# Kernel optimization log

Measured on AMD Instinct MI355X. Metric: run time of the kernel, lower is better.

The kernel has to match this reference:

```python
import jax, jax.numpy as jnp
import numpy as np

B, C, H, W, N = 16, 81, 128, 128, 64


def setup_inputs() -> dict:
    key = jax.random.key(0)
    k1, k2, k3, k4, k5 = jax.random.split(key, 5)
    bbox_pred = jax.random.normal(k1, (B, 4, H, W), jnp.float32)
    class_pred = jax.random.normal(k2, (B, C, H, W), jnp.float32)
    # well-formed GT boxes in [0,1]: x1y1 + positive wh
    xy = jax.random.uniform(k3, (B, N, 2), jnp.float32)
    wh = jax.random.uniform(k4, (B, N, 2), jnp.float32) * 0.5 + 0.05
    boxes = jnp.concatenate([xy, xy + wh], axis=-1)  # [B,N,4]
    labels = jax.random.randint(k5, (B, N), 0, C).astype(jnp.int32)
    return {"bbox_pred": bbox_pred, "class_pred": class_pred,
            "boxes": boxes, "labels": labels}


def reference(bbox_pred, class_pred, boxes, labels):
    Bb, Cc, Hh, Ww = class_pred.shape
    A = Hh * Ww
    pb = bbox_pred.transpose(0, 2, 3, 1).reshape(Bb, A, 4)   # [B,A,4]
    pc = class_pred.transpose(0, 2, 3, 1).reshape(Bb, A, Cc)  # [B,A,C]

    # pairwise IoU [B,A,N] via broadcasting (pred [B,A,1,4] vs gt [B,1,N,4])
    p = pb[:, :, None, :]
    g = boxes[:, None, :, :]
    ix1 = jnp.maximum(p[..., 0], g[..., 0])
    iy1 = jnp.maximum(p[..., 1], g[..., 1])
    ix2 = jnp.minimum(p[..., 2], g[..., 2])
    iy2 = jnp.minimum(p[..., 3], g[..., 3])
    inter = jnp.clip(ix2 - ix1, 0) * jnp.clip(iy2 - iy1, 0)
    pa = (pb[..., 2] - pb[..., 0]) * (pb[..., 3] - pb[..., 1])      # [B,A]
    ga = (boxes[..., 2] - boxes[..., 0]) * (boxes[..., 3] - boxes[..., 1])  # [B,N]
    union = pa[:, :, None] + ga[:, None, :] - inter
    ious = inter / union

    max_ious = ious.max(axis=-1)            # [B,A]
    max_idx = jnp.argmax(ious, axis=-1)     # [B,A]
    pos = max_ious > 0.5                    # [B,A]
    posf = pos.astype(pc.dtype)
    npos = posf.sum(axis=-1)                # [B]
    denom = jnp.maximum(npos, 1.0)

    assigned_labels = jnp.take_along_axis(labels, max_idx, axis=1)          # [B,A]
    assigned_boxes = jnp.take_along_axis(boxes, max_idx[..., None], axis=1)  # [B,A,4]

    # cross-entropy per anchor (mean over positives)
    logp = jax.nn.log_softmax(pc, axis=-1)
    ce = -jnp.take_along_axis(logp, assigned_labels[..., None], axis=2)[..., 0]
    cls_loss = (ce * posf).sum(axis=-1) / denom

    # smooth-L1 (beta=1), mean over positive elements (npos*4)
    diff = pb - assigned_boxes
    ad = jnp.abs(diff)
    sl1 = jnp.where(ad < 1.0, 0.5 * diff * diff, ad - 0.5)
    reg_loss = (sl1 * posf[..., None]).sum(axis=(-1, -2)) / (denom * 4.0)

    # fallback when an image has zero positives: CE with all-zero labels
    zero_loss = -logp[..., 0].mean(axis=-1)

    per_img = jnp.where(npos > 0, cls_loss + reg_loss, zero_loss)
    return per_img.mean()
```

## Files before the change

kernel.cpp:

```cpp
#include <hip/hip_runtime.h>
#include <math.h>

#define Bc 16
#define Cc 81
#define AA 16384
#define Nn 64
#define TPB 256
#define ILP 2
#define APB (TPB * ILP)
#define BLOCKS_PER_IMG (AA / APB)
#define NBLOCKS (Bc * BLOCKS_PER_IMG)
#define G 9
#define NG 9

__global__ __launch_bounds__(TPB) void det_loss_main(
    const float* __restrict__ bbox_pred,
    const float* __restrict__ class_pred,
    const float* __restrict__ boxes,
    const int* __restrict__ labels,
    float4* __restrict__ ws_part)
{
    __shared__ float4 sbox[Nn];
    __shared__ float  sga[Nn];
    __shared__ int    slab[Nn];

    const int blk  = blockIdx.x;
    const int b    = blk / BLOCKS_PER_IMG;
    const int ablk = blk % BLOCKS_PER_IMG;
    const int t    = threadIdx.x;

    if (t < Nn) {
        float4 g = ((const float4*)boxes)[b * Nn + t];
        sbox[t] = g;
        sga[t]  = (g.z - g.x) * (g.w - g.y);
        slab[t] = labels[b * Nn + t];
    }
    __syncthreads();

    const int a0 = ablk * APB + 2 * t;

    const float* bp = bbox_pred + (size_t)b * 4 * AA + a0;
    const float2 X1 = *(const float2*)(bp + 0 * AA);
    const float2 Y1 = *(const float2*)(bp + 1 * AA);
    const float2 X2 = *(const float2*)(bp + 2 * AA);
    const float2 Y2 = *(const float2*)(bp + 3 * AA);
    const float pa_0 = (X2.x - X1.x) * (Y2.x - Y1.x);
    const float pa_1 = (X2.y - X1.y) * (Y2.y - Y1.y);

    const float* cp = class_pred + (size_t)b * Cc * AA + a0;
    float2 buf0[G], buf1[G];
#pragma unroll
    for (int k = 0; k < G; ++k) buf0[k] = *(const float2*)(cp + (size_t)k * AA);

    float best0 = -INFINITY, best1 = -INFINITY;
    int   j0 = 0, j1 = 0;
#pragma unroll 8
    for (int j = 0; j < Nn; ++j) {
        const float4 g  = sbox[j];
        const float  ga = sga[j];
        {
            const float ix1 = fmaxf(X1.x, g.x);
            const float iy1 = fmaxf(Y1.x, g.y);
            const float ix2 = fminf(X2.x, g.z);
            const float iy2 = fminf(Y2.x, g.w);
            const float inter = fmaxf(ix2 - ix1, 0.0f) * fmaxf(iy2 - iy1, 0.0f);
            const float iou = inter * __builtin_amdgcn_rcpf(pa_0 + ga - inter);
            if (iou > best0) { best0 = iou; j0 = j; }
        }
        {
            const float ix1 = fmaxf(X1.y, g.x);
            const float iy1 = fmaxf(Y1.y, g.y);
            const float ix2 = fminf(X2.y, g.z);
            const float iy2 = fminf(Y2.y, g.w);
            const float inter = fmaxf(ix2 - ix1, 0.0f) * fmaxf(iy2 - iy1, 0.0f);
            const float iou = inter * __builtin_amdgcn_rcpf(pa_1 + ga - inter);
            if (iou > best1) { best1 = iou; j1 = j; }
        }
    }
    const float posf0 = (best0 > 0.5f) ? 1.0f : 0.0f;
    const float posf1 = (best1 > 0.5f) ? 1.0f : 0.0f;
    const int    lab0 = slab[j0];
    const int    lab1 = slab[j1];
    const float4 gb0  = sbox[j0];
    const float4 gb1  = sbox[j1];

    const float xl0 = class_pred[((size_t)b * Cc + lab0) * AA + a0];
    const float xl1 = class_pred[((size_t)b * Cc + lab1) * AA + a0 + 1];

    float sA0 = 0.0f, sA1 = 0.0f, sB0 = 0.0f, sB1 = 0.0f;
    float x00 = 0.0f, x01 = 0.0f;
#pragma unroll
    for (int g = 0; g < NG; ++g) {
        if (g + 1 < NG) {
            if ((g & 1) == 0) {
#pragma unroll
                for (int k = 0; k < G; ++k)
                    buf1[k] = *(const float2*)(cp + (size_t)((g + 1) * G + k) * AA);
            } else {
#pragma unroll
                for (int k = 0; k < G; ++k)
                    buf0[k] = *(const float2*)(cp + (size_t)((g + 1) * G + k) * AA);
            }
        }
#pragma unroll
        for (int k = 0; k < G; ++k) {
            const float2 x = ((g & 1) == 0) ? buf0[k] : buf1[k];
            if (g == 0 && k == 0) { x00 = x.x; x01 = x.y; }
            if (k & 1) { sB0 += __expf(x.x); sB1 += __expf(x.y); }
            else       { sA0 += __expf(x.x); sA1 += __expf(x.y); }
        }
    }
    const float lse0 = __logf(sA0 + sB0);
    const float lse1 = __logf(sA1 + sB1);

    const float ce    = (lse0 - xl0) * posf0 + (lse1 - xl1) * posf1;
    const float logp0 = (x00 - lse0) + (x01 - lse1);

    float sl = 0.0f;
    {
        const float d0 = X1.x - gb0.x, d1 = Y1.x - gb0.y, d2 = X2.x - gb0.z, d3 = Y2.x - gb0.w;
        const float a_0 = fabsf(d0), a_1 = fabsf(d1), a_2 = fabsf(d2), a_3 = fabsf(d3);
        float s0 = 0.0f;
        s0 += (a_0 < 1.0f) ? 0.5f * d0 * d0 : a_0 - 0.5f;
        s0 += (a_1 < 1.0f) ? 0.5f * d1 * d1 : a_1 - 0.5f;
        s0 += (a_2 < 1.0f) ? 0.5f * d2 * d2 : a_2 - 0.5f;
        s0 += (a_3 < 1.0f) ? 0.5f * d3 * d3 : a_3 - 0.5f;
        sl += s0 * posf0;
    }
    {
        const float d0 = X1.y - gb1.x, d1 = Y1.y - gb1.y, d2 = X2.y - gb1.z, d3 = Y2.y - gb1.w;
        const float a_0 = fabsf(d0), a_1 = fabsf(d1), a_2 = fabsf(d2), a_3 = fabsf(d3);
        float s1 = 0.0f;
        s1 += (a_0 < 1.0f) ? 0.5f * d0 * d0 : a_0 - 0.5f;
        s1 += (a_1 < 1.0f) ? 0.5f * d1 * d1 : a_1 - 0.5f;
        s1 += (a_2 < 1.0f) ? 0.5f * d2 * d2 : a_2 - 0.5f;
        s1 += (a_3 < 1.0f) ? 0.5f * d3 * d3 : a_3 - 0.5f;
        sl += s1 * posf1;
    }

    float v0 = posf0 + posf1, v1 = ce, v2 = sl, v3 = logp0;
#pragma unroll
    for (int o = 32; o > 0; o >>= 1) {
        v0 += __shfl_down(v0, o);
        v1 += __shfl_down(v1, o);
        v2 += __shfl_down(v2, o);
        v3 += __shfl_down(v3, o);
    }
    __shared__ float4 red[4];
    const int wave = t >> 6, lane = t & 63;
    if (lane == 0) red[wave] = make_float4(v0, v1, v2, v3);
    __syncthreads();
    if (t == 0) {
        float4 r0 = red[0], r1 = red[1], r2 = red[2], r3 = red[3];
        ws_part[blk] = make_float4(r0.x + r1.x + r2.x + r3.x,
                                   r0.y + r1.y + r2.y + r3.y,
                                   r0.z + r1.z + r2.z + r3.z,
                                   r0.w + r1.w + r2.w + r3.w);
    }
}

__global__ __launch_bounds__(256) void det_loss_final(
    const float4* __restrict__ ws_part, float* __restrict__ out)
{
    const int t = threadIdx.x;
    float4 p0 = ws_part[t];
    float4 p1 = ws_part[t + 256];
#pragma unroll
    for (int o = 1; o < 32; o <<= 1) {
        p0.x += __shfl_xor(p0.x, o); p0.y += __shfl_xor(p0.y, o);
        p0.z += __shfl_xor(p0.z, o); p0.w += __shfl_xor(p0.w, o);
        p1.x += __shfl_xor(p1.x, o); p1.y += __shfl_xor(p1.y, o);
        p1.z += __shfl_xor(p1.z, o); p1.w += __shfl_xor(p1.w, o);
    }
    __shared__ float4 simg[16];
    const int lane = t & 63, w = t >> 6;
    if (lane == 0 || lane == 32) {
        const int img = 2 * w + (lane >> 5);
        simg[img]     = p0;
        simg[img + 8] = p1;
    }
    __syncthreads();
    float per = 0.0f;
    if (t < Bc) {
        const float4 s = simg[t];
        const float npos = s.x;
        const float denom = fmaxf(npos, 1.0f);
        const float cls_reg = s.y / denom + s.z / (denom * 4.0f);
        const float zero_loss = -s.w / (float)AA;
        per = (npos > 0.0f) ? cls_reg : zero_loss;
    }
#pragma unroll
    for (int o = 8; o > 0; o >>= 1) per += __shfl_down(per, o);
    if (t == 0) out[0] = per * (1.0f / (float)Bc);
}

extern "C" void kernel_launch(void* const* d_in, const int* in_sizes, int n_in,
                              void* d_out, int out_size, void* d_ws, size_t ws_size,
                              hipStream_t stream) {
    const float* bbox_pred  = (const float*)d_in[0];
    const float* class_pred = (const float*)d_in[1];
    const float* boxes      = (const float*)d_in[2];
    const int*   labels     = (const int*)d_in[3];
    float* out = (float*)d_out;
    float4* ws = (float4*)d_ws;

    det_loss_main<<<NBLOCKS, TPB, 0, stream>>>(bbox_pred, class_pred, boxes, labels, ws);
    det_loss_final<<<1, 256, 0, stream>>>(ws, out);
}
```

Measured before the change: 25.14 us.

## Triple-buffer class loads, use nontemporal loads, select label logit in-loop

Deepens the class-logit prefetch from double to triple buffering, so two groups of channel loads are in flight while the IoU loop and exp sums run. All streaming loads become nontemporal. The separate gather of the assigned-label logit is replaced by a select inside the channel loop, which removes one dependent global load after the IoU search. The cost is more VGPRs for the third buffer plus extra compare/select work per channel, which could lower occupancy.

```diff
diff --git a/kernel.cpp b/kernel.cpp
--- a/kernel.cpp
+++ b/kernel.cpp
@@ -1,17 +1,26 @@
 #include <hip/hip_runtime.h>
 #include <math.h>
+#include <string.h>
 
 #define Bc 16
 #define Cc 81
 #define AA 16384
 #define Nn 64
 #define TPB 256
-#define ILP 2
-#define APB (TPB * ILP)
+#define APB 512
 #define BLOCKS_PER_IMG (AA / APB)
 #define NBLOCKS (Bc * BLOCKS_PER_IMG)
 #define G 9
 #define NG 9
+
+#define NTL(p) __builtin_nontemporal_load(p)
+
+__device__ __forceinline__ float2 ntl2(const float* p) {
+    const double d = __builtin_nontemporal_load((const double*)p);
+    float2 r;
+    memcpy(&r, &d, 8);
+    return r;
+}
 
 __global__ __launch_bounds__(TPB) void det_loss_main(
     const float* __restrict__ bbox_pred,
@@ -40,17 +49,19 @@
     const int a0 = ablk * APB + 2 * t;
 
     const float* bp = bbox_pred + (size_t)b * 4 * AA + a0;
-    const float2 X1 = *(const float2*)(bp + 0 * AA);
-    const float2 Y1 = *(const float2*)(bp + 1 * AA);
-    const float2 X2 = *(const float2*)(bp + 2 * AA);
-    const float2 Y2 = *(const float2*)(bp + 3 * AA);
-    const float pa_0 = (X2.x - X1.x) * (Y2.x - Y1.x);
-    const float pa_1 = (X2.y - X1.y) * (Y2.y - Y1.y);
+    const float2 X1 = ntl2(bp + 0 * AA);
+    const float2 Y1 = ntl2(bp + 1 * AA);
+    const float2 X2 = ntl2(bp + 2 * AA);
+    const float2 Y2 = ntl2(bp + 3 * AA);
+    const float pa0 = (X2.x - X1.x) * (Y2.x - Y1.x);
+    const float pa1 = (X2.y - X1.y) * (Y2.y - Y1.y);
 
     const float* cp = class_pred + (size_t)b * Cc * AA + a0;
-    float2 buf0[G], buf1[G];
-#pragma unroll
-    for (int k = 0; k < G; ++k) buf0[k] = *(const float2*)(cp + (size_t)k * AA);
+    float2 buf0[G], buf1[G], buf2[G];
+#pragma unroll
+    for (int k = 0; k < G; ++k) buf0[k] = ntl2(cp + (size_t)(0 * G + k) * AA);
+#pragma unroll
+    for (int k = 0; k < G; ++k) buf1[k] = ntl2(cp + (size_t)(1 * G + k) * AA);
 
     float best0 = -INFINITY, best1 = -INFINITY;
     int   j0 = 0, j1 = 0;
@@ -64,7 +75,7 @@
             const float ix2 = fminf(X2.x, g.z);
             const float iy2 = fminf(Y2.x, g.w);
             const float inter = fmaxf(ix2 - ix1, 0.0f) * fmaxf(iy2 - iy1, 0.0f);
-            const float iou = inter * __builtin_amdgcn_rcpf(pa_0 + ga - inter);
+            const float iou = inter * __builtin_amdgcn_rcpf(pa0 + ga - inter);
             if (iou > best0) { best0 = iou; j0 = j; }
         }
         {
@@ -73,7 +84,7 @@
             const float ix2 = fminf(X2.y, g.z);
             const float iy2 = fminf(Y2.y, g.w);
             const float inter = fmaxf(ix2 - ix1, 0.0f) * fmaxf(iy2 - iy1, 0.0f);
-            const float iou = inter * __builtin_amdgcn_rcpf(pa_1 + ga - inter);
+            const float iou = inter * __builtin_amdgcn_rcpf(pa1 + ga - inter);
             if (iou > best1) { best1 = iou; j1 = j; }
         }
     }
@@ -84,35 +95,40 @@
     const float4 gb0  = sbox[j0];
     const float4 gb1  = sbox[j1];
 
-    const float xl0 = class_pred[((size_t)b * Cc + lab0) * AA + a0];
-    const float xl1 = class_pred[((size_t)b * Cc + lab1) * AA + a0 + 1];
-
-    float sA0 = 0.0f, sA1 = 0.0f, sB0 = 0.0f, sB1 = 0.0f;
-    float x00 = 0.0f, x01 = 0.0f;
+    float sA0 = 0.0f, sB0 = 0.0f, sA1 = 0.0f, sB1 = 0.0f;
+    float x00 = 0.0f, x01 = 0.0f, xl0 = 0.0f, xl1 = 0.0f;
 #pragma unroll
     for (int g = 0; g < NG; ++g) {
-        if (g + 1 < NG) {
-            if ((g & 1) == 0) {
+        if (g + 2 < NG) {
+            const int m = (g + 2) % 3;
+            if (m == 0) {
 #pragma unroll
                 for (int k = 0; k < G; ++k)
-                    buf1[k] = *(const float2*)(cp + (size_t)((g + 1) * G + k) * AA);
+                    buf0[k] = ntl2(cp + (size_t)((g + 2) * G + k) * AA);
+            } else if (m == 1) {
+#pragma unroll
+                for (int k = 0; k < G; ++k)
+                    buf1[k] = ntl2(cp + (size_t)((g + 2) * G + k) * AA);
             } else {
 #pragma unroll
                 for (int k = 0; k < G; ++k)
-                    buf0[k] = *(const float2*)(cp + (size_t)((g + 1) * G + k) * AA);
+                    buf2[k] = ntl2(cp + (size_t)((g + 2) * G + k) * AA);
             }
         }
+        const int mc = g % 3;
 #pragma unroll
         for (int k = 0; k < G; ++k) {
-            const float2 x = ((g & 1) == 0) ? buf0[k] : buf1[k];
-            if (g == 0 && k == 0) { x00 = x.x; x01 = x.y; }
+            const float2 x = (mc == 0) ? buf0[k] : ((mc == 1) ? buf1[k] : buf2[k]);
+            const int    c = g * G + k;
+            if (c == 0) { x00 = x.x; x01 = x.y; }
+            xl0 = (c == lab0) ? x.x : xl0;
+            xl1 = (c == lab1) ? x.y : xl1;
             if (k & 1) { sB0 += __expf(x.x); sB1 += __expf(x.y); }
             else       { sA0 += __expf(x.x); sA1 += __expf(x.y); }
         }
     }
     const float lse0 = __logf(sA0 + sB0);
     const float lse1 = __logf(sA1 + sB1);
-
     const float ce    = (lse0 - xl0) * posf0 + (lse1 - xl1) * posf1;
     const float logp0 = (x00 - lse0) + (x01 - lse1);
 
```

Result: slower. 26.27 us (+4.5%).
